# Performance work log

Measured on AMD Instinct MI355X. Metric: run time of the kernel, lower is better.

The kernel has to match this reference:

```python
import jax, jax.numpy as jnp
from jax import lax
import numpy as np

B, T, D, H = 256, 256, 128, 256


def _lstm(x, Wih, Whh, bih, bhh):
    """Single-layer batch-first LSTM matching torch.nn.LSTM gate order (i,f,g,o).
    x: [B,T,Din]; Wih: [4Hout,Din]; Whh: [4Hout,Hout]; biases: [4Hout].
    Returns full hidden sequence [B,T,Hout]."""
    Hout = Whh.shape[1]
    # precompute input contributions for all timesteps in one big GEMM
    x_proj = jnp.einsum('btd,gd->btg', x, Wih) + bih + bhh  # [B,T,4H]

    def step(carry, xt):
        h, c = carry
        gates = xt + h @ Whh.T  # [B,4H]
        i, f, g, o = jnp.split(gates, 4, axis=-1)
        i = jax.nn.sigmoid(i)
        f = jax.nn.sigmoid(f)
        g = jnp.tanh(g)
        o = jax.nn.sigmoid(o)
        c = f * c + i * g
        h = o * jnp.tanh(c)
        return (h, c), h

    h0 = jnp.zeros((x.shape[0], Hout), x.dtype)
    (_, _), hs = lax.scan(step, (h0, h0), jnp.swapaxes(x_proj, 0, 1))
    return jnp.swapaxes(hs, 0, 1)  # [B,T,Hout]


def setup_inputs() -> dict:
    key = jax.random.key(0)
    ks = jax.random.split(key, 9)
    s_enc = 1.0 / np.sqrt(H)  # torch LSTM init scale (uniform bound); use scaled normal
    s_dec = 1.0 / np.sqrt(D)
    return {
        'x': jax.random.normal(ks[0], (B, T, D), jnp.float32),
        'enc_Wih': jax.random.normal(ks[1], (4 * H, D), jnp.float32) * s_enc,
        'enc_Whh': jax.random.normal(ks[2], (4 * H, H), jnp.float32) * s_enc,
        'enc_bih': jax.random.normal(ks[3], (4 * H,), jnp.float32) * s_enc,
        'enc_bhh': jax.random.normal(ks[4], (4 * H,), jnp.float32) * s_enc,
        'dec_Wih': jax.random.normal(ks[5], (4 * D, H), jnp.float32) * s_dec,
        'dec_Whh': jax.random.normal(ks[6], (4 * D, D), jnp.float32) * s_dec,
        'dec_bih': jax.random.normal(ks[7], (4 * D,), jnp.float32) * s_dec,
        'dec_bhh': jax.random.normal(ks[8], (4 * D,), jnp.float32) * s_dec,
    }


def reference(x, enc_Wih, enc_Whh, enc_bih, enc_bhh, dec_Wih, dec_Whh, dec_bih, dec_bhh):
    encoded = _lstm(x, enc_Wih, enc_Whh, enc_bih, enc_bhh)     # [B,T,H]
    decoded = _lstm(encoded, dec_Wih, dec_Whh, dec_bih, dec_bhh)  # [B,T,D]
    return decoded
```

## Files before the change

kernel.cpp:

```cpp
#include <hip/hip_runtime.h>
#include <stdint.h>


#define B_N 256
#define T_N 256
#define D_N 128
#define H_N 256

typedef __attribute__((ext_vector_type(8))) short bf16x8;
typedef __attribute__((ext_vector_type(4))) float f32x4;
typedef unsigned short u16;
typedef unsigned int u32;
typedef __attribute__((ext_vector_type(4))) u32 u32v4;

__device__ __forceinline__ float bflo(u32 u){ return __uint_as_float(u << 16); }
__device__ __forceinline__ float bfhi(u32 u){ return __uint_as_float(u & 0xffff0000u); }
__device__ __forceinline__ u32 f2bf_bits(float f){ u32 u = __float_as_uint(f); return (u + 0x7fffu + ((u >> 16) & 1u)) >> 16; }
__device__ __forceinline__ u32 pack2(float lo, float hi){ return f2bf_bits(lo) | (f2bf_bits(hi) << 16); }
__device__ __forceinline__ u32 cvtpk(float lo, float hi){ u32 r; asm("v_cvt_pk_bf16_f32 %0, %1, %2" : "=v"(r) : "v"(lo), "v"(hi)); return r; }
__device__ __forceinline__ float sigm(float x){ return __builtin_amdgcn_rcpf(1.f + __expf(-x)); }
__device__ __forceinline__ float tanh_f(float x){ return 1.f - 2.f * __builtin_amdgcn_rcpf(1.f + __expf(2.f * x)); }
template<int CTRL, int BANK>
__device__ __forceinline__ float pack_dpp(float oldv, float srcv){
  return __uint_as_float((u32)__builtin_amdgcn_update_dpp(
      (int)__float_as_uint(oldv), (int)__float_as_uint(srcv),
      CTRL, 0xF , BANK, false));
}

__global__ __launch_bounds__(256) void k_prep(
    const float* __restrict__ x, u16* __restrict__ xb,
    const float* __restrict__ eWih, u16* __restrict__ WihEp,
    const float* __restrict__ eWhh, u16* __restrict__ WhhEp,
    const float* __restrict__ dWih, u16* __restrict__ WihDp,
    const float* __restrict__ dWhh, u16* __restrict__ WhhDp,
    const float* __restrict__ ebih, const float* __restrict__ ebhh, float* __restrict__ bE,
    const float* __restrict__ dbih, const float* __restrict__ dbhh, float* __restrict__ bD){
  int blk = blockIdx.x;
  if (blk < 8192){
    const int i = (blk * 256 + threadIdx.x) * 4;
    float4 v = *(const float4*)(x + i);
    uint2 o; o.x = pack2(v.x, v.y); o.y = pack2(v.z, v.w);
    *(uint2*)(xb + i) = o;
    return;
  }
  blk -= 8192;
  const float* W; u16* Wp; int K, UB, VB = 3;
  if (blk < 1024){                 W = eWih; Wp = WihEp; K = 128; UB = 5; }
  else if (blk < 2048){ blk -= 1024; W = eWhh; Wp = WhhEp; K = 256; UB = 5; }
  else if (blk < 2560){ blk -= 2048; W = dWih; Wp = WihDp; K = 256; UB = 4; }
  else if (blk < 3072){ blk -= 2560; W = dWhh; Wp = WhhDp; K = 128; UB = 4; }
  else {
    blk -= 3072;
    const float* b1 = blk ? dbih : ebih;
    const float* b2 = blk ? dbhh : ebhh;
    float* bp = blk ? bD : bE;
    const int P = blk ? 512 : 1024, UBb = blk ? 4 : 5;
    for (int p = threadIdx.x; p < P; p += 256){
      int uo = p & ((1 << UBb) - 1), g = (p >> UBb) & 3, v = p >> (UBb + 2);
      int orig = (g << (UBb + 3)) | (v << UBb) | uo;
      bp[p] = b1[orig] + b2[orig];
    }
    return;
  }
  const int p = blk;
  const int uo = p & ((1 << UB) - 1), g = (p >> UB) & 3, v = p >> (UB + 2);
  const int orig = (g << (UB + VB)) | (v << UB) | uo;
  for (int k = threadIdx.x; k < K; k += 256)
    Wp[(size_t)p * K + k] = (u16)f2bf_bits(W[(size_t)orig * K + k]);
}

template<int KTOT, bool ENC_MAP, int UB, int VB, int SB>
__global__ __launch_bounds__(256, 1) void k_xproj(const u16* __restrict__ A, const u16* __restrict__ W,
                                                  const float* __restrict__ bias, u16* __restrict__ outp){
  constexpr int NQ  = 1 << (UB - 4);
  constexpr int NCH = 2 * NQ;
  constexpr size_t VS = (size_t)NCH * SB * 32;
  constexpr size_t WS = (size_t)(1 << VB) * VS;
  constexpr size_t TS = (size_t)(B_N / SB) * WS;
  __shared__ u16 As[64][72];
  __shared__ u16 Ws[64][72];
  const int tid = threadIdx.x, l = tid & 63, v = tid >> 6;
  const int lb = l & 15, lq = l >> 4;
  const int m0 = blockIdx.x * 64, n0 = blockIdx.y * 64;
  f32x4 acc[4];
#pragma unroll
  for (int nt = 0; nt < 4; nt++){ float bv = bias[n0 + nt * 16 + lb]; f32x4 t = {bv, bv, bv, bv}; acc[nt] = t; }
  const int r = tid >> 3, c8 = (tid & 7) * 8;
  for (int kb = 0; kb < KTOT / 64; ++kb){
    __syncthreads();
    *(bf16x8*)&As[r][c8]      = *(const bf16x8*)&A[(size_t)(m0 + r) * KTOT + kb * 64 + c8];
    *(bf16x8*)&As[r + 32][c8] = *(const bf16x8*)&A[(size_t)(m0 + r + 32) * KTOT + kb * 64 + c8];
    *(bf16x8*)&Ws[r][c8]      = *(const bf16x8*)&W[(size_t)(n0 + r) * KTOT + kb * 64 + c8];
    *(bf16x8*)&Ws[r + 32][c8] = *(const bf16x8*)&W[(size_t)(n0 + r + 32) * KTOT + kb * 64 + c8];
    __syncthreads();
#pragma unroll
    for (int kc = 0; kc < 2; kc++){
      bf16x8 af = *(const bf16x8*)&As[v * 16 + lb][kc * 32 + lq * 8];
#pragma unroll
      for (int nt = 0; nt < 4; nt++){
        bf16x8 wf = *(const bf16x8*)&Ws[nt * 16 + lb][kc * 32 + lq * 8];
        acc[nt] = __builtin_amdgcn_mfma_f32_16x16x32_bf16(af, wf, acc[nt], 0, 0, 0);
      }
    }
  }
#pragma unroll
  for (int nt = 0; nt < 4; nt++){
    const int n  = n0 + nt * 16 + lb;
    const int wv = n >> (UB + 2);
    const int g  = (n >> UB) & 3;
    const int w  = n & ((1 << UB) - 1);
    const int q  = w >> 4;
    const int u  = w & 15;
    const int qg = q * 4 + g;
    const size_t nbase = (size_t)wv * VS + (size_t)(qg >> 1) * (SB * 32) + (size_t)(u >> 2) * (SB * 8)
                       + (size_t)(qg & 1) * 4 + (size_t)(u & 3);
#pragma unroll
    for (int j = 0; j < 4; j += 2){
      const u32 pk = cvtpk(acc[nt][j], acc[nt][j + 1]);
#pragma unroll
      for (int s = 0; s < 2; ++s){
        const int m = m0 + v * 16 + lq * 4 + j + s;
        const int t = ENC_MAP ? (m & 255) : (m >> 8);
        const int b = ENC_MAP ? (m >> 8)  : (m & 255);
        outp[(size_t)t * TS + (size_t)(b / SB) * WS + (size_t)(b % SB) * 8 + nbase]
            = (u16)(s ? (pk >> 16) : (pk & 0xffffu));
      }
    }
  }
}

template<int KDIM, int NWAVE, int SB, int NMT, int NKC, int NQ, int F_REG, int F_LDS, bool IS_DEC>
__global__ __launch_bounds__(NWAVE * 64, NWAVE / 4)
void k_rec(const u16* __restrict__ Wp, const u16* __restrict__ xp,
           u16* __restrict__ enc_out, float* __restrict__ out){
  constexpr int BUFS = NKC * 512;
  constexpr int NCH = 2 * NQ;
  constexpr int CHS = SB * 32;
  constexpr size_t XSTR_T = (size_t)B_N * NWAVE * NCH * 32;
  static_assert(NMT == 4 * NQ, "tiles = 4 gates x NQ unit groups");
  static_assert(F_REG + F_LDS <= NMT * NKC, "reg+LDS tiers within total frags");
  extern __shared__ u16 smem[];
  u16* hbuf = smem;
  u16* al   = smem + 2 * BUFS;
  const int tid = threadIdx.x, l = tid & 63, v = tid >> 6;
  const int lb = l & 15, lq = l >> 4;
  const int b0 = blockIdx.x * SB;
  const u16* wwave = Wp + (size_t)(v * (NMT * 16) + lb) * KDIM + lq * 8;
  u16* alw = al + (size_t)v * F_LDS * 512;

  bf16x8 Areg[(F_REG > 0) ? F_REG : 1];
#pragma unroll
  for (int kc = 0; kc < NKC; ++kc)
#pragma unroll
    for (int mt = 0; mt < NMT; ++mt){
      const int idx = kc * NMT + mt;
      const u16* src = wwave + (size_t)(mt * 16) * KDIM + kc * 32;
      if (idx < F_REG)              Areg[idx] = *(const bf16x8*)src;
      else if (idx < F_REG + F_LDS) *(bf16x8*)&alw[(idx - F_REG) * 512 + l * 8] = *(const bf16x8*)src;
    }

  const u16* xpl = xp + ((size_t)blockIdx.x * NWAVE + v) * ((size_t)NCH * CHS) + lq * (SB * 8) + lb * 8;
  uint4 xq[NCH] = {};
  if (lb < SB){
#pragma unroll
    for (int i = 0; i < NCH; ++i) xq[i] = *(const uint4*)(xpl + (size_t)i * CHS);
  }

  for (int i = tid; i < 2 * BUFS; i += NWAVE * 64) hbuf[i] = 0;
  float c[4];
#pragma unroll
  for (int j = 0; j < 4; j++) c[j] = 0.f;
  __syncthreads();

  for (int t = 0; t < T_N; ++t){
    const u16* hrd = hbuf + (size_t)(t & 1) * BUFS;
    u16*       hwr = hbuf + (size_t)((t & 1) ^ 1) * BUFS;

    if constexpr (NQ == 2){
      f32x4 acc[2][4];
#pragma unroll
      for (int ph = 0; ph < 2; ++ph)
#pragma unroll
        for (int g = 0; g < 4; ++g){
          const int qg = ph * 4 + g;
          const uint4 cx = xq[qg >> 1];
          const u32 w0 = (qg & 1) ? cx.z : cx.x;
          const u32 w1 = (qg & 1) ? cx.w : cx.y;
          acc[ph][g][0] = bflo(w0); acc[ph][g][1] = bfhi(w0);
          acc[ph][g][2] = bflo(w1); acc[ph][g][3] = bfhi(w1);
        }
      if (t + 1 < T_N && lb < SB){
#pragma unroll
        for (int ch = 0; ch < NCH; ++ch)
          xq[ch] = *(const uint4*)(xpl + XSTR_T + (size_t)ch * CHS);
      }
      __builtin_amdgcn_s_setprio(1);
#pragma unroll
      for (int kc = 0; kc < NKC; ++kc){
        const bf16x8 bh = *(const bf16x8*)&hrd[kc * 512 + l * 8];
#pragma unroll
        for (int ph = 0; ph < 2; ++ph)
#pragma unroll
          for (int g = 0; g < 4; ++g){
            const int idx = kc * NMT + g * NQ + ph;
            bf16x8 af;
            if (idx < F_REG)              af = Areg[idx];
            else if (idx < F_REG + F_LDS) af = *(const bf16x8*)&alw[(idx - F_REG) * 512 + l * 8];
            else {
              const int mt = g * NQ + ph;
              u32v4 gw = *(const volatile u32v4*)(wwave + (size_t)(mt * 16) * KDIM + kc * 32);
              af = __builtin_bit_cast(bf16x8, gw);
            }
            acc[ph][g] = __builtin_amdgcn_mfma_f32_16x16x32_bf16(af, bh, acc[ph][g], 0, 0, 0);
          }
      }
      __builtin_amdgcn_s_setprio(0);
      if constexpr (SB == 8){
        f32x4 comb[4];
#pragma unroll
        for (int g = 0; g < 4; ++g)
#pragma unroll
          for (int j = 0; j < 4; ++j)
            comb[g][j] = pack_dpp<0x118, 0xC>(acc[0][g][j], acc[1][g][j]);
        float hv[4];
#pragma unroll
        for (int j = 0; j < 4; ++j){
          float iv = sigm(comb[0][j]);
          float fv = sigm(comb[1][j]);
          float gv = tanh_f(comb[2][j]);
          float ov = sigm(comb[3][j]);
          float cc = fv * c[j] + iv * gv;
          c[j] = cc;
          hv[j] = ov * tanh_f(cc);
        }
        const int u0 = v * 32 + (lb >> 3) * 16 + lq * 4;
        const int widx = (u0 >> 5) * 512 + ((u0 >> 3) & 3) * 128 + (lb & 7) * 8 + (u0 & 7);
        uint2 hp; hp.x = cvtpk(hv[0], hv[1]); hp.y = cvtpk(hv[2], hv[3]);
        *(uint2*)&hwr[widx] = hp;
        __syncthreads();
        *(uint2*)(enc_out + (size_t)(t * 256 + b0 + (lb & 7)) * KDIM + u0) = hp;
      } else {
        f32x4 comb[4];
#pragma unroll
        for (int g = 0; g < 4; ++g)
#pragma unroll
          for (int j = 0; j < 4; ++j)
            comb[g][j] = pack_dpp<0x114, 0x2>(acc[0][g][j], acc[1][g][j]);
        float fin[4][2];
#pragma unroll
        for (int g = 0; g < 4; ++g)
#pragma unroll
          for (int jj = 0; jj < 2; ++jj)
            fin[g][jj] = pack_dpp<0x118, 0xC>(comb[g][jj], comb[g][jj + 2]);
        float hv[2];
#pragma unroll
        for (int jj = 0; jj < 2; ++jj){
          float iv = sigm(fin[0][jj]);
          float fv = sigm(fin[1][jj]);
          float gv = tanh_f(fin[2][jj]);
          float ov = sigm(fin[3][jj]);
          float cc = fv * c[jj] + iv * gv;
          c[jj] = cc;
          hv[jj] = ov * tanh_f(cc);
        }
        const int bq = lb & 3, ph = (lb >> 2) & 1, jh = lb >> 3;
        const int u0 = v * 32 + ph * 16 + lq * 4 + jh * 2;
        const int widx = (u0 >> 5) * 512 + ((u0 >> 3) & 3) * 128 + bq * 8 + (u0 & 7);
        const u32 hp = cvtpk(hv[0], hv[1]);
        *(u32*)&hwr[widx] = hp;
        __syncthreads();
        *(u32*)(enc_out + (size_t)(t * 256 + b0 + bq) * KDIM + u0) = hp;
      }
    } else {
      float hv[2];
      int u0d;
      {
        const int q = 0;
        f32x4 acc[4];
#pragma unroll
        for (int g = 0; g < 4; ++g){
          const uint4 cx = xq[(q * 4 + g) >> 1];
          const u32 w0 = (g & 1) ? cx.z : cx.x;
          const u32 w1 = (g & 1) ? cx.w : cx.y;
          acc[g][0] = bflo(w0); acc[g][1] = bfhi(w0);
          acc[g][2] = bflo(w1); acc[g][3] = bfhi(w1);
        }
        if (t + 1 < T_N && lb < SB){
#pragma unroll
          for (int ch = 0; ch < NCH; ++ch)
            xq[ch] = *(const uint4*)(xpl + XSTR_T + (size_t)ch * CHS);
        }
        __builtin_amdgcn_s_setprio(1);
#pragma unroll
        for (int kc = 0; kc < NKC; ++kc){
          const bf16x8 bh = *(const bf16x8*)&hrd[kc * 512 + l * 8];
#pragma unroll
          for (int g = 0; g < 4; ++g){
            const int idx = kc * NMT + g * NQ + q;
            bf16x8 af;
            if (idx < F_REG)              af = Areg[idx];
            else if (idx < F_REG + F_LDS) af = *(const bf16x8*)&alw[(idx - F_REG) * 512 + l * 8];
            else {
              const int mt = g * NQ + q;
              u32v4 gw = *(const volatile u32v4*)(wwave + (size_t)(mt * 16) * KDIM + kc * 32);
              af = __builtin_bit_cast(bf16x8, gw);
            }
            acc[g] = __builtin_amdgcn_mfma_f32_16x16x32_bf16(af, bh, acc[g], 0, 0, 0);
          }
        }
        __builtin_amdgcn_s_setprio(0);
        float fin[4][2];
#pragma unroll
        for (int g = 0; g < 4; ++g)
#pragma unroll
          for (int jj = 0; jj < 2; ++jj)
            fin[g][jj] = pack_dpp<0x118, 0xC>(acc[g][jj], acc[g][jj + 2]);
#pragma unroll
        for (int jj = 0; jj < 2; ++jj){
          float iv = sigm(fin[0][jj]);
          float fv = sigm(fin[1][jj]);
          float gv = tanh_f(fin[2][jj]);
          float ov = sigm(fin[3][jj]);
          float cc = fv * c[jj] + iv * gv;
          c[jj] = cc;
          hv[jj] = ov * tanh_f(cc);
        }
        u0d = v * 16 + lq * 4 + (lb >> 3) * 2;
        const int widx = (u0d >> 5) * 512 + ((u0d >> 3) & 3) * 128 + (lb & 7) * 8 + (u0d & 7);
        const u32 hp = cvtpk(hv[0], hv[1]);
        *(u32*)&hwr[widx] = hp;
      }
      __syncthreads();
      {
        float2 o2; o2.x = hv[0]; o2.y = hv[1];
        *(float2*)(out + ((size_t)(b0 + (lb & 7)) * T_N + t) * D_N + u0d) = o2;
      }
    }
    xpl += XSTR_T;
  }
}

extern "C" void kernel_launch(void* const* d_in, const int* in_sizes, int n_in,
                              void* d_out, int out_size, void* d_ws, size_t ws_size,
                              hipStream_t stream){
  const float* x    = (const float*)d_in[0];
  const float* eWih = (const float*)d_in[1];
  const float* eWhh = (const float*)d_in[2];
  const float* ebih = (const float*)d_in[3];
  const float* ebhh = (const float*)d_in[4];
  const float* dWih = (const float*)d_in[5];
  const float* dWhh = (const float*)d_in[6];
  const float* dbih = (const float*)d_in[7];
  const float* dbhh = (const float*)d_in[8];
  float* out = (float*)d_out;

  char* w = (char*)d_ws;
  size_t off = 0;
  auto carve = [&](size_t bytes) -> void* { void* p = w + off; off = (off + bytes + 255) & ~(size_t)255; return p; };
  u16*   xb    = (u16*)carve((size_t)B_N * T_N * D_N * 2);
  u16*   WihEp = (u16*)carve((size_t)4 * H_N * D_N * 2);
  u16*   WhhEp = (u16*)carve((size_t)4 * H_N * H_N * 2);
  u16*   WihDp = (u16*)carve((size_t)4 * D_N * H_N * 2);
  u16*   WhhDp = (u16*)carve((size_t)4 * D_N * D_N * 2);
  float* bE    = (float*)carve((size_t)4 * H_N * 4);
  float* bD    = (float*)carve((size_t)4 * D_N * 4);
  u16*   xpE   = (u16*)carve((size_t)T_N * B_N * 4 * H_N * 2);
  u16*   enc   = (u16*)carve((size_t)T_N * B_N * H_N * 2);
  u16*   xpD   = (u16*)carve((size_t)T_N * B_N * 4 * D_N * 2);
  (void)ws_size; (void)in_sizes; (void)n_in; (void)out_size;

  hipLaunchKernelGGL(k_prep, dim3(8192 + 3072 + 2), dim3(256), 0, stream,
                     x, xb, eWih, WihEp, eWhh, WhhEp, dWih, WihDp, dWhh, WhhDp,
                     ebih, ebhh, bE, dbih, dbhh, bD);

  hipLaunchKernelGGL((k_xproj<128, true, 5, 3, 4>),  dim3(1024, 16), dim3(256), 0, stream, xb,  WihEp, bE, xpE);
  hipLaunchKernelGGL((k_rec<256, 8, 4, 8, 8, 2, 44, 18, false>), dim3(64), dim3(512),
                     2 * 8 * 512 * 2 + 8 * 18 * 1024, stream, WhhEp, xpE, enc, (float*)nullptr);
  hipLaunchKernelGGL((k_xproj<256, false, 4, 3, 8>), dim3(1024, 8),  dim3(256), 0, stream, enc, WihDp, bD, xpD);
  hipLaunchKernelGGL((k_rec<128, 8, 8, 4, 4, 1, 16, 0, true>),  dim3(32), dim3(512),
                     2 * 4 * 512 * 2, stream, WhhDp, xpD, (u16*)nullptr, out);
}
```

Before: 982.3 us.

## Transpose x to time-major in prep and stage xproj outputs through LDS

The prep kernel now writes the bf16 copy of x in time-major order, so every 64-row tile in the encoder input-projection GEMM belongs to a single timestep, the same as the decoder. This lets the projection kernel drop its per-element scattered 2-byte global stores. Results are written into a swizzled shared-memory staging buffer and then stored as contiguous 16-byte vectors in the recurrent kernel's layout. It adds an extra LDS pass, a sync and 8KB more shared memory per block in exchange for coalesced writes.

```diff
diff --git a/kernel.cpp b/kernel.cpp
--- a/kernel.cpp
+++ b/kernel.cpp
@@ -38,13 +38,15 @@
   int blk = blockIdx.x;
   if (blk < 8192){
     const int i = (blk * 256 + threadIdx.x) * 4;
+    const int d = i & 127, rest = i >> 7;
+    const int t = rest & 255, b = rest >> 8;
     float4 v = *(const float4*)(x + i);
     uint2 o; o.x = pack2(v.x, v.y); o.y = pack2(v.z, v.w);
-    *(uint2*)(xb + i) = o;
+    *(uint2*)(xb + (size_t)(t * 256 + b) * 128 + d) = o;
     return;
   }
   blk -= 8192;
-  const float* W; u16* Wp; int K, UB, VB = 3;
+  const float* W; u16* Wp; int K, UB;
   if (blk < 1024){                 W = eWih; Wp = WihEp; K = 128; UB = 5; }
   else if (blk < 2048){ blk -= 1024; W = eWhh; Wp = WhhEp; K = 256; UB = 5; }
   else if (blk < 2560){ blk -= 2048; W = dWih; Wp = WihDp; K = 256; UB = 4; }
@@ -64,12 +66,12 @@
   }
   const int p = blk;
   const int uo = p & ((1 << UB) - 1), g = (p >> UB) & 3, v = p >> (UB + 2);
-  const int orig = (g << (UB + VB)) | (v << UB) | uo;
+  const int orig = (g << (UB + 3)) | (v << UB) | uo;
   for (int k = threadIdx.x; k < K; k += 256)
     Wp[(size_t)p * K + k] = (u16)f2bf_bits(W[(size_t)orig * K + k]);
 }
 
-template<int KTOT, bool ENC_MAP, int UB, int VB, int SB>
+template<int KTOT, int UB, int VB, int SB>
 __global__ __launch_bounds__(256, 1) void k_xproj(const u16* __restrict__ A, const u16* __restrict__ W,
                                                   const float* __restrict__ bias, u16* __restrict__ outp){
   constexpr int NQ  = 1 << (UB - 4);
@@ -79,6 +81,7 @@
   constexpr size_t TS = (size_t)(B_N / SB) * WS;
   __shared__ u16 As[64][72];
   __shared__ u16 Ws[64][72];
+  __shared__ u16 ostage[4096];
   const int tid = threadIdx.x, l = tid & 63, v = tid >> 6;
   const int lb = l & 15, lq = l >> 4;
   const int m0 = blockIdx.x * 64, n0 = blockIdx.y * 64;
@@ -103,28 +106,53 @@
       }
     }
   }
+  __syncthreads();
 #pragma unroll
   for (int nt = 0; nt < 4; nt++){
-    const int n  = n0 + nt * 16 + lb;
-    const int wv = n >> (UB + 2);
-    const int g  = (n >> UB) & 3;
-    const int w  = n & ((1 << UB) - 1);
-    const int q  = w >> 4;
-    const int u  = w & 15;
-    const int qg = q * 4 + g;
-    const size_t nbase = (size_t)wv * VS + (size_t)(qg >> 1) * (SB * 32) + (size_t)(u >> 2) * (SB * 8)
-                       + (size_t)(qg & 1) * 4 + (size_t)(u & 3);
+    const int n = n0 + nt * 16 + lb;
+    const int u = lb;
+    int inner;
+    if constexpr (NQ == 1){
+      const int g = (n >> 4) & 3;
+      inner = (g >> 1) * 256 + (u >> 2) * 64 + (g & 1) * 4 + (u & 3);
+    } else {
+      const int q = (n >> 4) & 1, g = (n >> 5) & 3;
+      inner = q * 128 + (u >> 2) * 32 + (g & 1) * 4 + (u & 3);
+    }
 #pragma unroll
     for (int j = 0; j < 4; j += 2){
       const u32 pk = cvtpk(acc[nt][j], acc[nt][j + 1]);
 #pragma unroll
       for (int s = 0; s < 2; ++s){
-        const int m = m0 + v * 16 + lq * 4 + j + s;
-        const int t = ENC_MAP ? (m & 255) : (m >> 8);
-        const int b = ENC_MAP ? (m >> 8)  : (m & 255);
-        outp[(size_t)t * TS + (size_t)(b / SB) * WS + (size_t)(b % SB) * 8 + nbase]
-            = (u16)(s ? (pk >> 16) : (pk & 0xffffu));
-      }
+        const int bl_ = v * 16 + lq * 4 + j + s;
+        int loff;
+        if constexpr (NQ == 1) loff = (bl_ >> 3) * 512 + inner + (bl_ & 7) * 8;
+        else                   loff = (bl_ >> 2) * 256 + inner + (bl_ & 3) * 8;
+        loff ^= ((loff >> 6) & 7) << 3;
+        ostage[loff] = (u16)(s ? (pk >> 16) : (pk & 0xffffu));
+      }
+    }
+  }
+  __syncthreads();
+  {
+    const int t  = m0 >> 8, b0 = m0 & 255;
+    const int sl0 = (NQ == 1) ? (b0 >> 3) : (b0 >> 2);
+    const int wv  = (NQ == 1) ? blockIdx.y : (blockIdx.y >> 1);
+    const int cb  = blockIdx.y & 1;
+#pragma unroll
+    for (int it = 0; it < 2; ++it){
+      const int o = (it * 256 + tid) * 8;
+      const int loff = o ^ (((o >> 6) & 7) << 3);
+      const uint4 vdat = *(const uint4*)&ostage[loff];
+      size_t dst;
+      if constexpr (NQ == 1)
+        dst = (size_t)t * TS + (size_t)(sl0 + (o >> 9)) * WS + (size_t)wv * VS + (o & 511);
+      else {
+        const int rr = o & 255, q = rr >> 7, ww = rr & 127;
+        dst = (size_t)t * TS + (size_t)(sl0 + (o >> 8)) * WS + (size_t)wv * VS
+            + (size_t)(q * 2 + cb) * 128 + ww;
+      }
+      *(uint4*)(outp + dst) = vdat;
     }
   }
 }
@@ -373,10 +401,10 @@
                      x, xb, eWih, WihEp, eWhh, WhhEp, dWih, WihDp, dWhh, WhhDp,
                      ebih, ebhh, bE, dbih, dbhh, bD);
 
-  hipLaunchKernelGGL((k_xproj<128, true, 5, 3, 4>),  dim3(1024, 16), dim3(256), 0, stream, xb,  WihEp, bE, xpE);
+  hipLaunchKernelGGL((k_xproj<128, 5, 3, 4>),  dim3(1024, 16), dim3(256), 0, stream, xb,  WihEp, bE, xpE);
   hipLaunchKernelGGL((k_rec<256, 8, 4, 8, 8, 2, 44, 18, false>), dim3(64), dim3(512),
                      2 * 8 * 512 * 2 + 8 * 18 * 1024, stream, WhhEp, xpE, enc, (float*)nullptr);
-  hipLaunchKernelGGL((k_xproj<256, false, 4, 3, 8>), dim3(1024, 8),  dim3(256), 0, stream, enc, WihDp, bD, xpD);
+  hipLaunchKernelGGL((k_xproj<256, 4, 3, 8>), dim3(1024, 8),  dim3(256), 0, stream, enc, WihDp, bD, xpD);
   hipLaunchKernelGGL((k_rec<128, 8, 8, 4, 4, 1, 16, 0, true>),  dim3(32), dim3(512),
                      2 * 4 * 512 * 2, stream, WhhDp, xpD, (u16*)nullptr, out);
 }
```

After: 912.1 us. -7.2%, faster.
